# Kernel optimization log

Measured on AMD Instinct MI355X. Metric: run time of the kernel, lower is better.

Reference implementation:

```python
import jax, jax.numpy as jnp
import numpy as np

N_HEAD = 16
D_IN = 1024
D_OUT = 1024
B, T = 2, 2048
HEAD_DIM = D_OUT // N_HEAD


def setup_inputs() -> dict:
    key = jax.random.key(0)
    ks = jax.random.split(key, 8)
    Q = jax.random.normal(ks[0], (B, T, D_IN), dtype=jnp.float32)
    K = jax.random.normal(ks[1], (B, T, D_IN), dtype=jnp.float32)
    V = jax.random.normal(ks[2], (B, T, D_IN), dtype=jnp.float32)
    mask = jax.random.randint(ks[3], (B, T, T), 0, 2, dtype=jnp.int32)
    s_in = 1.0 / np.sqrt(D_IN)
    s_out = 1.0 / np.sqrt(D_OUT)
    Wq = jax.random.uniform(ks[4], (D_IN, D_OUT), jnp.float32, -s_in, s_in)
    Wk = jax.random.uniform(ks[5], (D_IN, D_OUT), jnp.float32, -s_in, s_in)
    Wv = jax.random.uniform(ks[6], (D_IN, D_OUT), jnp.float32, -s_in, s_in)
    Wo = jax.random.uniform(ks[7], (D_OUT, D_OUT), jnp.float32, -s_out, s_out)
    return {"Q": Q, "K": K, "V": V, "mask": mask,
            "Wq": Wq, "Wk": Wk, "Wv": Wv, "Wo": Wo}


def _split_heads(x):
    b, t, _ = x.shape
    return x.reshape(b, t, N_HEAD, HEAD_DIM).transpose(0, 2, 1, 3)  # [B,H,T,hd]


def reference(Q, K, V, mask, Wq, Wk, Wv, Wo):
    q = _split_heads(Q @ Wq)
    k = _split_heads(K @ Wk)
    v = _split_heads(V @ Wv)
    scale = 1.0 / jnp.sqrt(jnp.float32(HEAD_DIM))  # Q.size(-1) after head split
    scores = jnp.einsum('bhqd,bhkd->bhqk', q, k) * scale  # [B,H,T,T]
    m = mask[:, None, :, :]  # expand over heads
    scores = jnp.where(m == 0, jnp.float32(-1e9), scores)
    attn = jax.nn.softmax(scores, axis=-1)
    z = jnp.einsum('bhqk,bhkd->bhqd', attn, v)  # [B,H,T,hd]
    z = z.transpose(0, 2, 1, 3).reshape(Q.shape[0], T, D_OUT)
    return z @ Wo
```

## Files before the change

### kernel.cpp

```cpp
#include <hip/hip_runtime.h>
#include <math.h>

#define DIN 1024
#define DOUT 1024
#define NHEAD 16
#define HDIM 64
#define BATCH 2
#define TSEQ 2048
#define MROWS (BATCH * TSEQ)

typedef unsigned short u16;
typedef __attribute__((ext_vector_type(8))) short short8;
typedef __attribute__((ext_vector_type(4))) float f32x4;
typedef __attribute__((ext_vector_type(4))) unsigned short us4;

__device__ __forceinline__ void f32_to_bf16pair(float x, u16& hi, u16& lo) {
  unsigned u = __float_as_uint(x);
  unsigned r = (u + 0x7fffu + ((u >> 16) & 1u)) & 0xffff0000u;
  hi = (u16)(r >> 16);
  float rem = x - __uint_as_float(r);
  unsigned u2 = __float_as_uint(rem);
  lo = (u16)((u2 + 0x7fffu + ((u2 >> 16) & 1u)) >> 16);
}

__device__ __forceinline__ void gld_lds16(const void* g, void* l) {
  __builtin_amdgcn_global_load_lds(
      (__attribute__((address_space(1))) void*)g,
      (__attribute__((address_space(3))) void*)l, 16, 0, 0);
}

__global__ __launch_bounds__(256) void splitA(
    const float* __restrict__ S0, const float* __restrict__ S1,
    const float* __restrict__ S2, u16* __restrict__ H0, u16* __restrict__ L0,
    u16* __restrict__ H1, u16* __restrict__ L1, u16* __restrict__ H2,
    u16* __restrict__ L2) {
  const int z = blockIdx.y;
  const float* S = z == 0 ? S0 : z == 1 ? S1 : S2;
  u16* H = z == 0 ? H0 : z == 1 ? H1 : H2;
  u16* L = z == 0 ? L0 : z == 1 ? L1 : L2;
  const size_t i = ((size_t)blockIdx.x * 256 + threadIdx.x) * 4;
  float4 v = *(const float4*)&S[i];
  us4 h4, l4;
  u16 hh, ll;
  f32_to_bf16pair(v.x, hh, ll);
  h4[0] = hh; l4[0] = ll;
  f32_to_bf16pair(v.y, hh, ll);
  h4[1] = hh; l4[1] = ll;
  f32_to_bf16pair(v.z, hh, ll);
  h4[2] = hh; l4[2] = ll;
  f32_to_bf16pair(v.w, hh, ll);
  h4[3] = hh; l4[3] = ll;
  *(us4*)&H[i] = h4;
  *(us4*)&L[i] = l4;
}

__global__ __launch_bounds__(256) void splitWt(
    const float* __restrict__ W0, const float* __restrict__ W1,
    const float* __restrict__ W2, const float* __restrict__ W3,
    u16* __restrict__ H0, u16* __restrict__ L0, u16* __restrict__ H1,
    u16* __restrict__ L1, u16* __restrict__ H2, u16* __restrict__ L2,
    u16* __restrict__ H3, u16* __restrict__ L3) {
  const int z = blockIdx.z;
  const float* W = z == 0 ? W0 : z == 1 ? W1 : z == 2 ? W2 : W3;
  u16* H = z == 0 ? H0 : z == 1 ? H1 : z == 2 ? H2 : H3;
  u16* L = z == 0 ? L0 : z == 1 ? L1 : z == 2 ? L2 : L3;
  __shared__ float ts[64][68];
  const int tid = threadIdx.x;
  const int k0 = blockIdx.y * 64, n0 = blockIdx.x * 64;
  {
    const int kl = tid >> 2, nc = (tid & 3) * 16;
#pragma unroll
    for (int c = 0; c < 4; ++c)
      *(float4*)&ts[kl][nc + c * 4] =
          *(const float4*)&W[(size_t)(k0 + kl) * DOUT + n0 + nc + c * 4];
  }
  __syncthreads();
  const int nl = tid >> 2, kc = (tid & 3) * 16;
#pragma unroll
  for (int g = 0; g < 4; ++g) {
    us4 h4, l4;
#pragma unroll
    for (int j = 0; j < 4; ++j) {
      u16 hh, ll;
      f32_to_bf16pair(ts[kc + g * 4 + j][nl], hh, ll);
      h4[j] = hh;
      l4[j] = ll;
    }
    const size_t idx = (size_t)(n0 + nl) * DIN + k0 + kc + g * 4;
    *(us4*)&H[idx] = h4;
    *(us4*)&L[idx] = l4;
  }
}

struct GemmPtrs {
  const u16* Ah;
  const u16* Al;
  const u16* Bh;
  const u16* Bl;
  u16* Oh;
  u16* Ol;
  float* Of;
  int mode;
};
struct GemmArgs {
  GemmPtrs p[3];
};

__global__ __launch_bounds__(256) void gemm_bf16(GemmArgs args) {
  const GemmPtrs P = args.p[blockIdx.z];
  __shared__ alignas(16) u16 Abuf[128 * 64];
  __shared__ alignas(16) u16 Bbuf[128 * 64];
  const int tid = threadIdx.x;
  const int w = tid >> 6, lane = tid & 63;
  const int lr = lane & 15, qd = lane >> 4;
  const int mw = w >> 1, nw = w & 1;
  const int n0 = blockIdx.x * 128, m0 = blockIdx.y * 128;

  const u16* gA[4];
  const u16* gB[4];
  u16* lA[4];
  u16* lB[4];
  {
    const int cl = lane & 7;
#pragma unroll
    for (int is = 0; is < 4; ++is) {
      const int row = is * 32 + w * 8 + (lane >> 3);
      const int cg = cl ^ (row & 7);
      gA[is] = (cg < 4 ? P.Ah : P.Al) + (size_t)(m0 + row) * DIN + (cg & 3) * 8;
      gB[is] = (cg < 4 ? P.Bh : P.Bl) + (size_t)(n0 + row) * DIN + (cg & 3) * 8;
      lA[is] = Abuf + (size_t)(is * 32 + w * 8) * 64;
      lB[is] = Bbuf + (size_t)(is * 32 + w * 8) * 64;
    }
  }

  f32x4 acc[4][4] = {};

  for (int kt = 0; kt < 32; ++kt) {
    __syncthreads();
#pragma unroll
    for (int is = 0; is < 4; ++is) {
      gld_lds16(gA[is], lA[is]);
      gld_lds16(gB[is], lB[is]);
      gA[is] += 32;
      gB[is] += 32;
    }
    __syncthreads();

    short8 af[4][2], bf[4][2];
#pragma unroll
    for (int t = 0; t < 4; ++t) {
      const int ra = mw * 64 + t * 16 + lr;
      af[t][0] = *(const short8*)&Abuf[ra * 64 + ((qd ^ (ra & 7)) << 3)];
      af[t][1] = *(const short8*)&Abuf[ra * 64 + (((qd + 4) ^ (ra & 7)) << 3)];
      const int rb = nw * 64 + t * 16 + lr;
      bf[t][0] = *(const short8*)&Bbuf[rb * 64 + ((qd ^ (rb & 7)) << 3)];
      bf[t][1] = *(const short8*)&Bbuf[rb * 64 + (((qd + 4) ^ (rb & 7)) << 3)];
    }
#pragma unroll
    for (int mt = 0; mt < 4; ++mt)
#pragma unroll
      for (int nt = 0; nt < 4; ++nt) {
        acc[mt][nt] = __builtin_amdgcn_mfma_f32_16x16x32_bf16(
            af[mt][0], bf[nt][0], acc[mt][nt], 0, 0, 0);
        acc[mt][nt] = __builtin_amdgcn_mfma_f32_16x16x32_bf16(
            af[mt][0], bf[nt][1], acc[mt][nt], 0, 0, 0);
        acc[mt][nt] = __builtin_amdgcn_mfma_f32_16x16x32_bf16(
            af[mt][1], bf[nt][0], acc[mt][nt], 0, 0, 0);
      }
  }

#pragma unroll
  for (int mt = 0; mt < 4; ++mt)
#pragma unroll
    for (int nt = 0; nt < 4; ++nt)
#pragma unroll
      for (int r = 0; r < 4; ++r) {
        const float val = acc[mt][nt][r];
        const int gm = m0 + mw * 64 + mt * 16 + qd * 4 + r;
        const int gn = n0 + nw * 64 + nt * 16 + lr;
        if (P.mode == 1) {
          P.Of[(size_t)gm * DOUT + gn] = val;
        } else {
          u16 hh16, ll16;
          f32_to_bf16pair(val, hh16, ll16);
          const int bb = gm >> 11, t = gm & 2047;
          const int h = gn >> 6, d = gn & 63;
          size_t idx;
          if (P.mode == 0)
            idx = (((size_t)(bb * NHEAD + h) * TSEQ) + t) * HDIM + d;
          else
            idx = (((size_t)(bb * NHEAD + h) * HDIM) + d) * TSEQ + t;
          P.Oh[idx] = hh16;
          P.Ol[idx] = ll16;
        }
      }
}

template <int MODE>
__global__ __launch_bounds__(256) void gemm64(const float* __restrict__ A,
                                              const float* __restrict__ W,
                                              void* __restrict__ Y0,
                                              void* __restrict__ Y1) {
  __shared__ float As[16][68];
  __shared__ float Bs[16][68];
  const int tid = threadIdx.x;
  const int tx = tid & 15, ty = tid >> 4;
  const int r0 = ty * 4, c0 = tx * 4;
  const int gm0 = blockIdx.x * 64;
  const int gn0 = blockIdx.y * 64;
  const int am = tid >> 2;
  const int ak0 = (tid & 3) * 4;
  const int bk = tid >> 4;
  const int bc = (tid & 15) * 4;
  float acc[4][4] = {};
  for (int k0 = 0; k0 < DIN; k0 += 16) {
    __syncthreads();
    alignas(16) float av[4];
    *(float4*)av = *(const float4*)&A[(size_t)(gm0 + am) * DIN + k0 + ak0];
    As[ak0 + 0][am] = av[0];
    As[ak0 + 1][am] = av[1];
    As[ak0 + 2][am] = av[2];
    As[ak0 + 3][am] = av[3];
    *(float4*)&Bs[bk][bc] = *(const float4*)&W[(size_t)(k0 + bk) * DOUT + gn0 + bc];
    __syncthreads();
#pragma unroll
    for (int kk = 0; kk < 16; ++kk) {
      alignas(16) float a[4], b[4];
      *(float4*)a = *(const float4*)&As[kk][r0];
      *(float4*)b = *(const float4*)&Bs[kk][c0];
#pragma unroll
      for (int i = 0; i < 4; ++i)
#pragma unroll
        for (int j = 0; j < 4; ++j) acc[i][j] += a[i] * b[j];
    }
  }
  if constexpr (MODE == 1) {
    float* Y = (float*)Y0;
#pragma unroll
    for (int i = 0; i < 4; ++i) {
      float4 o = make_float4(acc[i][0], acc[i][1], acc[i][2], acc[i][3]);
      *(float4*)&Y[(size_t)(gm0 + r0 + i) * DOUT + gn0 + c0] = o;
    }
  } else if constexpr (MODE == 0) {
    u16* Yh = (u16*)Y0;
    u16* Yl = (u16*)Y1;
    const int bb = gm0 >> 11, tb = gm0 & 2047, h = gn0 >> 6;
#pragma unroll
    for (int i = 0; i < 4; ++i) {
      us4 h4, l4;
#pragma unroll
      for (int j = 0; j < 4; ++j) {
        u16 hh, ll;
        f32_to_bf16pair(acc[i][j], hh, ll);
        h4[j] = hh;
        l4[j] = ll;
      }
      size_t idx = (((size_t)(bb * NHEAD + h) * TSEQ) + tb + r0 + i) * HDIM + c0;
      *(us4*)&Yh[idx] = h4;
      *(us4*)&Yl[idx] = l4;
    }
  } else {
    __shared__ float ts[64][68];
#pragma unroll
    for (int i = 0; i < 4; ++i) {
      float4 o = make_float4(acc[i][0], acc[i][1], acc[i][2], acc[i][3]);
      *(float4*)&ts[r0 + i][c0] = o;
    }
    __syncthreads();
    u16* Yh = (u16*)Y0;
    u16* Yl = (u16*)Y1;
    const int bb = gm0 >> 11, tb = gm0 & 2047, h = gn0 >> 6;
    const int d = tid >> 2;
    const int t0 = (tid & 3) * 16;
#pragma unroll
    for (int g = 0; g < 4; ++g) {
      us4 h4, l4;
#pragma unroll
      for (int j = 0; j < 4; ++j) {
        u16 hh, ll;
        f32_to_bf16pair(ts[t0 + g * 4 + j][d], hh, ll);
        h4[j] = hh;
        l4[j] = ll;
      }
      size_t idx = (((size_t)(bb * NHEAD + h) * HDIM) + d) * TSEQ + tb + t0 + g * 4;
      *(us4*)&Yh[idx] = h4;
      *(us4*)&Yl[idx] = l4;
    }
  }
}

template <int EPI>
__global__ __launch_bounds__(256) void attn_mfma(
    const u16* __restrict__ qh, const u16* __restrict__ ql,
    const u16* __restrict__ kh, const u16* __restrict__ kl,
    const u16* __restrict__ vh, const u16* __restrict__ vl,
    const int* __restrict__ mask, float* __restrict__ zf,
    u16* __restrict__ zh, u16* __restrict__ zl) {
  __shared__ alignas(16) u16 lds_k[2][64 * 64];
  __shared__ alignas(16) u16 lds_v[2][64 * 64];
  __shared__ alignas(16) u16 lds_p[4][32 * 64];
  const int tid = threadIdx.x;
  const int w = tid >> 6, lane = tid & 63;
  const int lr = lane & 15, qd = lane >> 4;
  const int bh = blockIdx.y;
  const int bb = bh >> 4, hh = bh & 15;
  const int qt0 = blockIdx.x * 128;
  const int wq0 = qt0 + w * 32;
  const size_t bh_off = (size_t)bh * TSEQ * HDIM;

  short8 qf[2][2][2];
#pragma unroll
  for (int mt = 0; mt < 2; ++mt)
#pragma unroll
    for (int ks = 0; ks < 2; ++ks) {
      const size_t off =
          bh_off + (size_t)(wq0 + mt * 16 + lr) * HDIM + ks * 32 + qd * 8;
      qf[mt][ks][0] = *(const short8*)(qh + off);
      qf[mt][ks][1] = *(const short8*)(ql + off);
    }

  f32x4 zacc[2][4] = {};
  float lsum[2][4] = {};

  const u16* stage_src = (w == 0 ? kh : w == 1 ? kl : w == 2 ? vh : vl) + bh_off;
  u16* stage_dst = (w < 2) ? &lds_k[w][0] : &lds_v[w - 2][0];
  const bool stage_is_k = (w < 2);

  for (int kt0 = 0; kt0 < TSEQ; kt0 += 64) {
    __syncthreads();
#pragma unroll
    for (int i = 0; i < 8; ++i) {
      const int c = i * 64 + lane;
      const int row = c >> 3;
      const int cc = c & 7;
      const u16* src = stage_is_k
                           ? stage_src + (size_t)(kt0 + row) * HDIM + cc * 8
                           : stage_src + (size_t)row * TSEQ + kt0 + cc * 8;
      uint4 dv = *(const uint4*)src;
      *(uint4*)&stage_dst[row * 64 + ((cc ^ (row & 7)) << 3)] = dv;
    }
    __syncthreads();

    int mv[2][4][4];
#pragma unroll
    for (int mt = 0; mt < 2; ++mt)
#pragma unroll
      for (int r = 0; r < 4; ++r) {
        const int qrow = wq0 + mt * 16 + qd * 4 + r;
        const size_t mb = ((size_t)bb * TSEQ + qrow) * TSEQ + kt0 + lr;
#pragma unroll
        for (int nt = 0; nt < 4; ++nt) mv[mt][nt][r] = mask[mb + nt * 16];
      }

    f32x4 sacc[2][4] = {};
#pragma unroll
    for (int ks = 0; ks < 2; ++ks)
#pragma unroll
      for (int nt = 0; nt < 4; ++nt) {
        const int krow = nt * 16 + lr;
        const int chunk = (((ks * 4 + qd) ^ (krow & 7)) << 3);
        short8 bhf = *(const short8*)&lds_k[0][krow * 64 + chunk];
        short8 blf = *(const short8*)&lds_k[1][krow * 64 + chunk];
#pragma unroll
        for (int mt = 0; mt < 2; ++mt) {
          sacc[mt][nt] = __builtin_amdgcn_mfma_f32_16x16x32_bf16(
              qf[mt][ks][0], bhf, sacc[mt][nt], 0, 0, 0);
          sacc[mt][nt] = __builtin_amdgcn_mfma_f32_16x16x32_bf16(
              qf[mt][ks][0], blf, sacc[mt][nt], 0, 0, 0);
          sacc[mt][nt] = __builtin_amdgcn_mfma_f32_16x16x32_bf16(
              qf[mt][ks][1], bhf, sacc[mt][nt], 0, 0, 0);
        }
      }

    u16* pw = &lds_p[w][0];
#pragma unroll
    for (int mt = 0; mt < 2; ++mt)
#pragma unroll
      for (int nt = 0; nt < 4; ++nt)
#pragma unroll
        for (int r = 0; r < 4; ++r) {
          float s = sacc[mt][nt][r];
          s = mv[mt][nt][r] ? s * 0.125f : -1.0e9f;
          float p = __expf(s);
          unsigned u = (__float_as_uint(p) + 0x8000u) & 0xffff0000u;
          lsum[mt][r] += __uint_as_float(u);
          const int prow = mt * 16 + qd * 4 + r;
          const int pcol = nt * 16 + lr;
          pw[prow * 64 + ((((pcol >> 3) ^ (prow & 7)) << 3)) + (pcol & 7)] =
              (u16)(u >> 16);
        }

#pragma unroll
    for (int ks = 0; ks < 2; ++ks) {
      short8 pf[2];
#pragma unroll
      for (int mt = 0; mt < 2; ++mt) {
        const int prow = mt * 16 + lr;
        const int chunk = (((ks * 4 + qd) ^ (prow & 7)) << 3);
        pf[mt] = *(const short8*)&pw[prow * 64 + chunk];
      }
#pragma unroll
      for (int nt = 0; nt < 4; ++nt) {
        const int vrow = nt * 16 + lr;
        const int chunk = (((ks * 4 + qd) ^ (vrow & 7)) << 3);
        short8 vhf = *(const short8*)&lds_v[0][vrow * 64 + chunk];
        short8 vlf = *(const short8*)&lds_v[1][vrow * 64 + chunk];
#pragma unroll
        for (int mt = 0; mt < 2; ++mt) {
          zacc[mt][nt] = __builtin_amdgcn_mfma_f32_16x16x32_bf16(
              pf[mt], vhf, zacc[mt][nt], 0, 0, 0);
          zacc[mt][nt] = __builtin_amdgcn_mfma_f32_16x16x32_bf16(
              pf[mt], vlf, zacc[mt][nt], 0, 0, 0);
        }
      }
    }
  }

#pragma unroll
  for (int mt = 0; mt < 2; ++mt)
#pragma unroll
    for (int r = 0; r < 4; ++r) {
      float v = lsum[mt][r];
#pragma unroll
      for (int off = 1; off < 16; off <<= 1) v += __shfl_xor(v, off);
      lsum[mt][r] = 1.0f / v;
    }
#pragma unroll
  for (int mt = 0; mt < 2; ++mt)
#pragma unroll
    for (int r = 0; r < 4; ++r) {
      const int qrow = wq0 + mt * 16 + qd * 4 + r;
      const float inv = lsum[mt][r];
#pragma unroll
      for (int nt = 0; nt < 4; ++nt) {
        const float val = zacc[mt][nt][r] * inv;
        const size_t idx =
            ((size_t)bb * TSEQ + qrow) * DOUT + hh * HDIM + nt * 16 + lr;
        if (EPI == 0) {
          zf[idx] = val;
        } else {
          u16 hh16, ll16;
          f32_to_bf16pair(val, hh16, ll16);
          zh[idx] = hh16;
          zl[idx] = ll16;
        }
      }
    }
}

extern "C" void kernel_launch(void* const* d_in, const int* in_sizes, int n_in,
                              void* d_out, int out_size, void* d_ws,
                              size_t ws_size, hipStream_t stream) {
  const float* Q = (const float*)d_in[0];
  const float* K = (const float*)d_in[1];
  const float* V = (const float*)d_in[2];
  const int* mask = (const int*)d_in[3];
  const float* Wq = (const float*)d_in[4];
  const float* Wk = (const float*)d_in[5];
  const float* Wv = (const float*)d_in[6];
  const float* Wo = (const float*)d_in[7];
  float* out = (float*)d_out;
  dim3 blk(256);

  if (ws_size >= (size_t)134217728) {
    u16* base = (u16*)d_ws;
    auto U = [&](size_t mib) { return base + mib * 524288; };
    u16 *Qh = U(0), *Ql = U(8), *Kh = U(16), *Kl = U(24), *Vh = U(32),
        *Vl = U(40);
    u16 *Wqh = U(48), *Wql = U(50), *Wkh = U(52), *Wkl = U(54), *Wvh = U(56),
        *Wvl = U(58), *Woh = U(60), *Wol = U(62);
    u16 *qh = U(64), *ql = U(72), *kh = U(80), *kl = U(88), *vth = U(96),
        *vtl = U(104);
    u16 *zh = U(112), *zl = U(120);

    splitA<<<dim3(4096, 3), blk, 0, stream>>>(Q, K, V, Qh, Ql, Kh, Kl, Vh, Vl);
    splitWt<<<dim3(16, 16, 4), blk, 0, stream>>>(Wq, Wk, Wv, Wo, Wqh, Wql, Wkh,
                                                 Wkl, Wvh, Wvl, Woh, Wol);
    GemmArgs ga;
    ga.p[0] = {Qh, Ql, Wqh, Wql, qh, ql, nullptr, 0};
    ga.p[1] = {Kh, Kl, Wkh, Wkl, kh, kl, nullptr, 0};
    ga.p[2] = {Vh, Vl, Wvh, Wvl, vth, vtl, nullptr, 2};
    gemm_bf16<<<dim3(8, 32, 3), blk, 0, stream>>>(ga);
    attn_mfma<1><<<dim3(TSEQ / 128, BATCH * NHEAD), blk, 0, stream>>>(
        qh, ql, kh, kl, vth, vtl, mask, nullptr, zh, zl);
    GemmArgs go;
    go.p[0] = {zh, zl, Woh, Wol, nullptr, nullptr, out, 1};
    go.p[1] = go.p[0];
    go.p[2] = go.p[0];
    gemm_bf16<<<dim3(8, 32, 1), blk, 0, stream>>>(go);
  } else {
    const size_t NE = (size_t)MROWS * DOUT;
    u16* qhb = (u16*)d_ws;
    u16* qlb = qhb + NE;
    u16* khb = qlb + NE;
    u16* klb = khb + NE;
    u16* vth = klb + NE;
    u16* vtl = vth + NE;
    float* zb = (float*)(vtl + NE);
    dim3 gg(MROWS / 64, DOUT / 64);
    gemm64<0><<<gg, blk, 0, stream>>>(Q, Wq, qhb, qlb);
    gemm64<0><<<gg, blk, 0, stream>>>(K, Wk, khb, klb);
    gemm64<2><<<gg, blk, 0, stream>>>(V, Wv, vth, vtl);
    attn_mfma<0><<<dim3(TSEQ / 128, BATCH * NHEAD), blk, 0, stream>>>(
        qhb, qlb, khb, klb, vth, vtl, mask, zb, nullptr, nullptr);
    gemm64<1><<<gg, blk, 0, stream>>>(zb, Wo, (void*)out, nullptr);
  }
}
```

Measured before the change: 477.1 us.

## Shrink attention query tile to 64 rows and split output GEMM along K

The attention kernel now gives each block 64 query rows (16 per wave) instead of 128, which doubles the grid to 1024 blocks. It also remaps block indices so neighbouring blocks share batch-heads, and stages K/V into LDS with direct global-to-LDS loads, with a 4-block occupancy hint. The output projection is split into two K-halves that write separate fp32 buffers, and a small sumC kernel adds them. This is meant to improve occupancy and fill more CUs on the 256-block launches, at the cost of more K/V re-reads per query, extra fp32 traffic, and one more launch.

```diff
diff --git a/kernel.cpp b/kernel.cpp
--- a/kernel.cpp
+++ b/kernel.cpp
@@ -99,14 +99,13 @@
   const u16* Bl;
   u16* Oh;
   u16* Ol;
-  float* Of;
   int mode;
 };
 struct GemmArgs {
   GemmPtrs p[3];
 };
 
-__global__ __launch_bounds__(256) void gemm_bf16(GemmArgs args) {
+__global__ __launch_bounds__(256) void gemm_qkv(GemmArgs args) {
   const GemmPtrs P = args.p[blockIdx.z];
   __shared__ alignas(16) u16 Abuf[128 * 64];
   __shared__ alignas(16) u16 Bbuf[128 * 64];
@@ -178,22 +177,106 @@
         const float val = acc[mt][nt][r];
         const int gm = m0 + mw * 64 + mt * 16 + qd * 4 + r;
         const int gn = n0 + nw * 64 + nt * 16 + lr;
-        if (P.mode == 1) {
-          P.Of[(size_t)gm * DOUT + gn] = val;
-        } else {
-          u16 hh16, ll16;
-          f32_to_bf16pair(val, hh16, ll16);
-          const int bb = gm >> 11, t = gm & 2047;
-          const int h = gn >> 6, d = gn & 63;
-          size_t idx;
-          if (P.mode == 0)
-            idx = (((size_t)(bb * NHEAD + h) * TSEQ) + t) * HDIM + d;
-          else
-            idx = (((size_t)(bb * NHEAD + h) * HDIM) + d) * TSEQ + t;
-          P.Oh[idx] = hh16;
-          P.Ol[idx] = ll16;
-        }
-      }
+        u16 hh16, ll16;
+        f32_to_bf16pair(val, hh16, ll16);
+        const int bb = gm >> 11, t = gm & 2047;
+        const int h = gn >> 6, d = gn & 63;
+        size_t idx;
+        if (P.mode == 0)
+          idx = (((size_t)(bb * NHEAD + h) * TSEQ) + t) * HDIM + d;
+        else
+          idx = (((size_t)(bb * NHEAD + h) * HDIM) + d) * TSEQ + t;
+        P.Oh[idx] = hh16;
+        P.Ol[idx] = ll16;
+      }
+}
+
+__global__ __launch_bounds__(256) void gemm_out(
+    const u16* __restrict__ Ah, const u16* __restrict__ Al,
+    const u16* __restrict__ Bh, const u16* __restrict__ Bl,
+    float* __restrict__ C0, float* __restrict__ C1) {
+  float* Of = blockIdx.z == 0 ? C0 : C1;
+  const int koff = blockIdx.z * 512;
+  __shared__ alignas(16) u16 Abuf[128 * 64];
+  __shared__ alignas(16) u16 Bbuf[128 * 64];
+  const int tid = threadIdx.x;
+  const int w = tid >> 6, lane = tid & 63;
+  const int lr = lane & 15, qd = lane >> 4;
+  const int mw = w >> 1, nw = w & 1;
+  const int n0 = blockIdx.x * 128, m0 = blockIdx.y * 128;
+
+  const u16* gA[4];
+  const u16* gB[4];
+  u16* lA[4];
+  u16* lB[4];
+  {
+    const int cl = lane & 7;
+#pragma unroll
+    for (int is = 0; is < 4; ++is) {
+      const int row = is * 32 + w * 8 + (lane >> 3);
+      const int cg = cl ^ (row & 7);
+      gA[is] = (cg < 4 ? Ah : Al) + (size_t)(m0 + row) * DIN + (cg & 3) * 8 + koff;
+      gB[is] = (cg < 4 ? Bh : Bl) + (size_t)(n0 + row) * DIN + (cg & 3) * 8 + koff;
+      lA[is] = Abuf + (size_t)(is * 32 + w * 8) * 64;
+      lB[is] = Bbuf + (size_t)(is * 32 + w * 8) * 64;
+    }
+  }
+
+  f32x4 acc[4][4] = {};
+
+  for (int kt = 0; kt < 16; ++kt) {
+    __syncthreads();
+#pragma unroll
+    for (int is = 0; is < 4; ++is) {
+      gld_lds16(gA[is], lA[is]);
+      gld_lds16(gB[is], lB[is]);
+      gA[is] += 32;
+      gB[is] += 32;
+    }
+    __syncthreads();
+
+    short8 af[4][2], bf[4][2];
+#pragma unroll
+    for (int t = 0; t < 4; ++t) {
+      const int ra = mw * 64 + t * 16 + lr;
+      af[t][0] = *(const short8*)&Abuf[ra * 64 + ((qd ^ (ra & 7)) << 3)];
+      af[t][1] = *(const short8*)&Abuf[ra * 64 + (((qd + 4) ^ (ra & 7)) << 3)];
+      const int rb = nw * 64 + t * 16 + lr;
+      bf[t][0] = *(const short8*)&Bbuf[rb * 64 + ((qd ^ (rb & 7)) << 3)];
+      bf[t][1] = *(const short8*)&Bbuf[rb * 64 + (((qd + 4) ^ (rb & 7)) << 3)];
+    }
+#pragma unroll
+    for (int mt = 0; mt < 4; ++mt)
+#pragma unroll
+      for (int nt = 0; nt < 4; ++nt) {
+        acc[mt][nt] = __builtin_amdgcn_mfma_f32_16x16x32_bf16(
+            af[mt][0], bf[nt][0], acc[mt][nt], 0, 0, 0);
+        acc[mt][nt] = __builtin_amdgcn_mfma_f32_16x16x32_bf16(
+            af[mt][0], bf[nt][1], acc[mt][nt], 0, 0, 0);
+        acc[mt][nt] = __builtin_amdgcn_mfma_f32_16x16x32_bf16(
+            af[mt][1], bf[nt][0], acc[mt][nt], 0, 0, 0);
+      }
+  }
+
+#pragma unroll
+  for (int mt = 0; mt < 4; ++mt)
+#pragma unroll
+    for (int nt = 0; nt < 4; ++nt)
+#pragma unroll
+      for (int r = 0; r < 4; ++r) {
+        const int gm = m0 + mw * 64 + mt * 16 + qd * 4 + r;
+        const int gn = n0 + nw * 64 + nt * 16 + lr;
+        Of[(size_t)gm * DOUT + gn] = acc[mt][nt][r];
+      }
+}
+
+__global__ __launch_bounds__(256) void sumC(const float* __restrict__ A,
+                                            const float* __restrict__ B,
+                                            float* __restrict__ O) {
+  const size_t i = ((size_t)blockIdx.x * 256 + threadIdx.x) * 4;
+  float4 a = *(const float4*)&A[i];
+  float4 b = *(const float4*)&B[i];
+  *(float4*)&O[i] = make_float4(a.x + b.x, a.y + b.y, a.z + b.z, a.w + b.w);
 }
 
 template <int MODE>
@@ -290,7 +373,7 @@
 }
 
 template <int EPI>
-__global__ __launch_bounds__(256) void attn_mfma(
+__global__ __launch_bounds__(256, 4) void attn64q(
     const u16* __restrict__ qh, const u16* __restrict__ ql,
     const u16* __restrict__ kh, const u16* __restrict__ kl,
     const u16* __restrict__ vh, const u16* __restrict__ vl,
@@ -298,61 +381,55 @@
     u16* __restrict__ zh, u16* __restrict__ zl) {
   __shared__ alignas(16) u16 lds_k[2][64 * 64];
   __shared__ alignas(16) u16 lds_v[2][64 * 64];
-  __shared__ alignas(16) u16 lds_p[4][32 * 64];
+  __shared__ alignas(16) u16 lds_p[4][16 * 64];
   const int tid = threadIdx.x;
   const int w = tid >> 6, lane = tid & 63;
   const int lr = lane & 15, qd = lane >> 4;
-  const int bh = blockIdx.y;
+  const int L = blockIdx.x;
+  const int bh = (L & 7) + 8 * ((L >> 3) & 3);
+  const int qt0 = (L >> 5) * 64;
   const int bb = bh >> 4, hh = bh & 15;
-  const int qt0 = blockIdx.x * 128;
-  const int wq0 = qt0 + w * 32;
+  const int wq0 = qt0 + w * 16;
   const size_t bh_off = (size_t)bh * TSEQ * HDIM;
 
-  short8 qf[2][2][2];
-#pragma unroll
-  for (int mt = 0; mt < 2; ++mt)
-#pragma unroll
-    for (int ks = 0; ks < 2; ++ks) {
-      const size_t off =
-          bh_off + (size_t)(wq0 + mt * 16 + lr) * HDIM + ks * 32 + qd * 8;
-      qf[mt][ks][0] = *(const short8*)(qh + off);
-      qf[mt][ks][1] = *(const short8*)(ql + off);
-    }
-
-  f32x4 zacc[2][4] = {};
-  float lsum[2][4] = {};
-
-  const u16* stage_src = (w == 0 ? kh : w == 1 ? kl : w == 2 ? vh : vl) + bh_off;
-  u16* stage_dst = (w < 2) ? &lds_k[w][0] : &lds_v[w - 2][0];
-  const bool stage_is_k = (w < 2);
+  short8 qf[2][2];
+#pragma unroll
+  for (int ks = 0; ks < 2; ++ks) {
+    const size_t off = bh_off + (size_t)(wq0 + lr) * HDIM + ks * 32 + qd * 8;
+    qf[ks][0] = *(const short8*)(qh + off);
+    qf[ks][1] = *(const short8*)(ql + off);
+  }
+
+  f32x4 zacc[4] = {};
+  float lsum[4] = {};
+
+  const u16* ssrc = (w == 0 ? kh : w == 1 ? kl : w == 2 ? vh : vl) + bh_off;
+  u16* sdst = (w < 2) ? &lds_k[w][0] : &lds_v[w - 2][0];
+  const bool isk = (w < 2);
+  const int srow = lane >> 3, scl = lane & 7;
+  const int* mrow = mask + ((size_t)bb * TSEQ + wq0 + qd * 4) * TSEQ + lr;
 
   for (int kt0 = 0; kt0 < TSEQ; kt0 += 64) {
     __syncthreads();
 #pragma unroll
-    for (int i = 0; i < 8; ++i) {
-      const int c = i * 64 + lane;
-      const int row = c >> 3;
-      const int cc = c & 7;
-      const u16* src = stage_is_k
-                           ? stage_src + (size_t)(kt0 + row) * HDIM + cc * 8
-                           : stage_src + (size_t)row * TSEQ + kt0 + cc * 8;
-      uint4 dv = *(const uint4*)src;
-      *(uint4*)&stage_dst[row * 64 + ((cc ^ (row & 7)) << 3)] = dv;
-    }
-    __syncthreads();
-
-    int mv[2][4][4];
-#pragma unroll
-    for (int mt = 0; mt < 2; ++mt)
-#pragma unroll
-      for (int r = 0; r < 4; ++r) {
-        const int qrow = wq0 + mt * 16 + qd * 4 + r;
-        const size_t mb = ((size_t)bb * TSEQ + qrow) * TSEQ + kt0 + lr;
-#pragma unroll
-        for (int nt = 0; nt < 4; ++nt) mv[mt][nt][r] = mask[mb + nt * 16];
-      }
-
-    f32x4 sacc[2][4] = {};
+    for (int is = 0; is < 8; ++is) {
+      const int row = is * 8 + srow;
+      const int cg = scl ^ (row & 7);
+      const u16* src = isk ? ssrc + (size_t)(kt0 + row) * HDIM + cg * 8
+                           : ssrc + (size_t)row * TSEQ + kt0 + cg * 8;
+      gld_lds16(src, sdst + is * 512);
+    }
+    __syncthreads();
+
+    int mv[4][4];
+#pragma unroll
+    for (int r = 0; r < 4; ++r) {
+      const int* mr = mrow + (size_t)r * TSEQ + kt0;
+#pragma unroll
+      for (int nt = 0; nt < 4; ++nt) mv[nt][r] = mr[nt * 16];
+    }
+
+    f32x4 sacc[4] = {};
 #pragma unroll
     for (int ks = 0; ks < 2; ++ks)
 #pragma unroll
@@ -361,91 +438,73 @@
         const int chunk = (((ks * 4 + qd) ^ (krow & 7)) << 3);
         short8 bhf = *(const short8*)&lds_k[0][krow * 64 + chunk];
         short8 blf = *(const short8*)&lds_k[1][krow * 64 + chunk];
-#pragma unroll
-        for (int mt = 0; mt < 2; ++mt) {
-          sacc[mt][nt] = __builtin_amdgcn_mfma_f32_16x16x32_bf16(
-              qf[mt][ks][0], bhf, sacc[mt][nt], 0, 0, 0);
-          sacc[mt][nt] = __builtin_amdgcn_mfma_f32_16x16x32_bf16(
-              qf[mt][ks][0], blf, sacc[mt][nt], 0, 0, 0);
-          sacc[mt][nt] = __builtin_amdgcn_mfma_f32_16x16x32_bf16(
-              qf[mt][ks][1], bhf, sacc[mt][nt], 0, 0, 0);
-        }
+        sacc[nt] = __builtin_amdgcn_mfma_f32_16x16x32_bf16(qf[ks][0], bhf,
+                                                           sacc[nt], 0, 0, 0);
+        sacc[nt] = __builtin_amdgcn_mfma_f32_16x16x32_bf16(qf[ks][0], blf,
+                                                           sacc[nt], 0, 0, 0);
+        sacc[nt] = __builtin_amdgcn_mfma_f32_16x16x32_bf16(qf[ks][1], bhf,
+                                                           sacc[nt], 0, 0, 0);
       }
 
     u16* pw = &lds_p[w][0];
 #pragma unroll
-    for (int mt = 0; mt < 2; ++mt)
-#pragma unroll
-      for (int nt = 0; nt < 4; ++nt)
-#pragma unroll
-        for (int r = 0; r < 4; ++r) {
-          float s = sacc[mt][nt][r];
-          s = mv[mt][nt][r] ? s * 0.125f : -1.0e9f;
-          float p = __expf(s);
-          unsigned u = (__float_as_uint(p) + 0x8000u) & 0xffff0000u;
-          lsum[mt][r] += __uint_as_float(u);
-          const int prow = mt * 16 + qd * 4 + r;
-          const int pcol = nt * 16 + lr;
-          pw[prow * 64 + ((((pcol >> 3) ^ (prow & 7)) << 3)) + (pcol & 7)] =
-              (u16)(u >> 16);
-        }
+    for (int nt = 0; nt < 4; ++nt)
+#pragma unroll
+      for (int r = 0; r < 4; ++r) {
+        float s = sacc[nt][r];
+        s = mv[nt][r] ? s * 0.125f : -1.0e9f;
+        float p = __expf(s);
+        unsigned u = (__float_as_uint(p) + 0x8000u) & 0xffff0000u;
+        lsum[r] += __uint_as_float(u);
+        const int prow = qd * 4 + r;
+        const int pcol = nt * 16 + lr;
+        pw[prow * 64 + ((((pcol >> 3) ^ (prow & 7)) << 3)) + (pcol & 7)] =
+            (u16)(u >> 16);
+      }
 
 #pragma unroll
     for (int ks = 0; ks < 2; ++ks) {
-      short8 pf[2];
-#pragma unroll
-      for (int mt = 0; mt < 2; ++mt) {
-        const int prow = mt * 16 + lr;
-        const int chunk = (((ks * 4 + qd) ^ (prow & 7)) << 3);
-        pf[mt] = *(const short8*)&pw[prow * 64 + chunk];
-      }
+      const int chunkp = (((ks * 4 + qd) ^ (lr & 7)) << 3);
+      short8 pf = *(const short8*)&pw[lr * 64 + chunkp];
 #pragma unroll
       for (int nt = 0; nt < 4; ++nt) {
         const int vrow = nt * 16 + lr;
         const int chunk = (((ks * 4 + qd) ^ (vrow & 7)) << 3);
         short8 vhf = *(const short8*)&lds_v[0][vrow * 64 + chunk];
         short8 vlf = *(const short8*)&lds_v[1][vrow * 64 + chunk];
-#pragma unroll
-        for (int mt = 0; mt < 2; ++mt) {
-          zacc[mt][nt] = __builtin_amdgcn_mfma_f32_16x16x32_bf16(
-              pf[mt], vhf, zacc[mt][nt], 0, 0, 0);
-          zacc[mt][nt] = __builtin_amdgcn_mfma_f32_16x16x32_bf16(
-              pf[mt], vlf, zacc[mt][nt], 0, 0, 0);
-        }
-      }
-    }
-  }
-
-#pragma unroll
-  for (int mt = 0; mt < 2; ++mt)
-#pragma unroll
-    for (int r = 0; r < 4; ++r) {
-      float v = lsum[mt][r];
-#pragma unroll
-      for (int off = 1; off < 16; off <<= 1) v += __shfl_xor(v, off);
-      lsum[mt][r] = 1.0f / v;
-    }
-#pragma unroll
-  for (int mt = 0; mt < 2; ++mt)
-#pragma unroll
-    for (int r = 0; r < 4; ++r) {
-      const int qrow = wq0 + mt * 16 + qd * 4 + r;
-      const float inv = lsum[mt][r];
-#pragma unroll
-      for (int nt = 0; nt < 4; ++nt) {
-        const float val = zacc[mt][nt][r] * inv;
-        const size_t idx =
-            ((size_t)bb * TSEQ + qrow) * DOUT + hh * HDIM + nt * 16 + lr;
-        if (EPI == 0) {
-          zf[idx] = val;
-        } else {
-          u16 hh16, ll16;
-          f32_to_bf16pair(val, hh16, ll16);
-          zh[idx] = hh16;
-          zl[idx] = ll16;
-        }
-      }
-    }
+        zacc[nt] = __builtin_amdgcn_mfma_f32_16x16x32_bf16(pf, vhf, zacc[nt],
+                                                           0, 0, 0);
+        zacc[nt] = __builtin_amdgcn_mfma_f32_16x16x32_bf16(pf, vlf, zacc[nt],
+                                                           0, 0, 0);
+      }
+    }
+  }
+
+#pragma unroll
+  for (int r = 0; r < 4; ++r) {
+    float v = lsum[r];
+#pragma unroll
+    for (int off = 1; off < 16; off <<= 1) v += __shfl_xor(v, off);
+    lsum[r] = 1.0f / v;
+  }
+#pragma unroll
+  for (int r = 0; r < 4; ++r) {
+    const int qrow = wq0 + qd * 4 + r;
+#pragma unroll
+    for (int nt = 0; nt < 4; ++nt) {
+      const float val = zacc[nt][r] * lsum[r];
+      const size_t idx =
+          ((size_t)bb * TSEQ + qrow) * DOUT + hh * HDIM + nt * 16 + lr;
+      if (EPI == 0) {
+        zf[idx] = val;
+      } else {
+        u16 hh16, ll16;
+        f32_to_bf16pair(val, hh16, ll16);
+        zh[idx] = hh16;
+        zl[idx] = ll16;
+      }
+    }
+  }
 }
 
 extern "C" void kernel_launch(void* const* d_in, const int* in_sizes, int n_in,
@@ -472,22 +531,21 @@
     u16 *qh = U(64), *ql = U(72), *kh = U(80), *kl = U(88), *vth = U(96),
         *vtl = U(104);
     u16 *zh = U(112), *zl = U(120);
+    float* C0 = (float*)U(0);
+    float* C1 = (float*)U(16);
 
     splitA<<<dim3(4096, 3), blk, 0, stream>>>(Q, K, V, Qh, Ql, Kh, Kl, Vh, Vl);
     splitWt<<<dim3(16, 16, 4), blk, 0, stream>>>(Wq, Wk, Wv, Wo, Wqh, Wql, Wkh,
                                                  Wkl, Wvh, Wvl, Woh, Wol);
     GemmArgs ga;
-    ga.p[0] = {Qh, Ql, Wqh, Wql, qh, ql, nullptr, 0};
-    ga.p[1] = {Kh, Kl, Wkh, Wkl, kh, kl, nullptr, 0};
-    ga.p[2] = {Vh, Vl, Wvh, Wvl, vth, vtl, nullptr, 2};
-    gemm_bf16<<<dim3(8, 32, 3), blk, 0, stream>>>(ga);
-    attn_mfma<1><<<dim3(TSEQ / 128, BATCH * NHEAD), blk, 0, stream>>>(
-        qh, ql, kh, kl, vth, vtl, mask, nullptr, zh, zl);
-    GemmArgs go;
-    go.p[0] = {zh, zl, Woh, Wol, nullptr, nullptr, out, 1};
-    go.p[1] = go.p[0];
-    go.p[2] = go.p[0];
-    gemm_bf16<<<dim3(8, 32, 1), blk, 0, stream>>>(go);
+    ga.p[0] = {Qh, Ql, Wqh, Wql, qh, ql, 0};
+    ga.p[1] = {Kh, Kl, Wkh, Wkl, kh, kl, 0};
+    ga.p[2] = {Vh, Vl, Wvh, Wvl, vth, vtl, 2};
+    gemm_qkv<<<dim3(8, 32, 3), blk, 0, stream>>>(ga);
+    attn64q<1><<<dim3(1024), blk, 0, stream>>>(qh, ql, kh, kl, vth, vtl, mask,
+                                               nullptr, zh, zl);
+    gemm_out<<<dim3(8, 32, 2), blk, 0, stream>>>(zh, zl, Woh, Wol, C0, C1);
+    sumC<<<dim3(4096), blk, 0, stream>>>(C0, C1, out);
   } else {
     const size_t NE = (size_t)MROWS * DOUT;
     u16* qhb = (u16*)d_ws;
@@ -501,8 +559,8 @@
     gemm64<0><<<gg, blk, 0, stream>>>(Q, Wq, qhb, qlb);
     gemm64<0><<<gg, blk, 0, stream>>>(K, Wk, khb, klb);
     gemm64<2><<<gg, blk, 0, stream>>>(V, Wv, vth, vtl);
-    attn_mfma<0><<<dim3(TSEQ / 128, BATCH * NHEAD), blk, 0, stream>>>(
-        qhb, qlb, khb, klb, vth, vtl, mask, zb, nullptr, nullptr);
+    attn64q<0><<<dim3(1024), blk, 0, stream>>>(qhb, qlb, khb, klb, vth, vtl,
+                                               mask, zb, nullptr, nullptr);
     gemm64<1><<<gg, blk, 0, stream>>>(zb, Wo, (void*)out, nullptr);
   }
 }
```

After: 409.6 us. 1.16x faster.
